# Performance work log

Hardware: AMD Instinct MI355X
Metric: run time of the kernel (lower is better)

The kernel has to match this reference:

```python
import jax, jax.numpy as jnp
import numpy as np

N = 50000
E = 800000
IN_DIM = 128
HIDDEN = 128
OUT_DIM = 64
NUM_GRAPHS = 64


def setup_inputs() -> dict:
    key = jax.random.key(0)
    ks = jax.random.split(key, 16)
    x = jax.random.normal(ks[0], (N, IN_DIM), dtype=jnp.float32)
    edge_index = jax.random.randint(ks[1], (2, E), 0, N, dtype=jnp.int32)
    batch = jnp.sort(jax.random.randint(ks[2], (N,), 0, NUM_GRAPHS, dtype=jnp.int32))

    def glorot(k, shape):
        fan_in = shape[1]
        return jax.random.normal(k, shape, dtype=jnp.float32) / jnp.sqrt(jnp.float32(fan_in))

    # SAGEConv params: lin_l (on aggregated neighbors, with bias), lin_r (on self, no bias)
    return {
        "x": x,
        "edge_index": edge_index,
        "batch": batch,
        "W1l": glorot(ks[3], (HIDDEN, IN_DIM)), "b1l": jnp.zeros((HIDDEN,), jnp.float32),
        "W1r": glorot(ks[4], (HIDDEN, IN_DIM)),
        "W2l": glorot(ks[5], (HIDDEN, HIDDEN)), "b2l": jnp.zeros((HIDDEN,), jnp.float32),
        "W2r": glorot(ks[6], (HIDDEN, HIDDEN)),
        "W3l": glorot(ks[7], (HIDDEN, HIDDEN)), "b3l": jnp.zeros((HIDDEN,), jnp.float32),
        "W3r": glorot(ks[8], (HIDDEN, HIDDEN)),
        "Wlin": glorot(ks[9], (OUT_DIM, HIDDEN)), "blin": jnp.zeros((OUT_DIM,), jnp.float32),
    }


def sage_conv(x, src, dst, Wl, bl, Wr):
    # aggr='add': scatter-add source features onto target nodes, then two linears.
    agg = jax.ops.segment_sum(x[src], dst, num_segments=N)  # [N, d_in]
    return agg @ Wl.T + bl + x @ Wr.T


def reference(x, edge_index, batch, W1l, b1l, W1r, W2l, b2l, W2r, W3l, b3l, W3r, Wlin, blin):
    src, dst = edge_index[0], edge_index[1]
    h = jax.nn.relu(sage_conv(x, src, dst, W1l, b1l, W1r))
    # dropout p=0.3 is identity at inference
    h = jax.nn.relu(sage_conv(h, src, dst, W2l, b2l, W2r))
    h = sage_conv(h, src, dst, W3l, b3l, W3r)
    # global mean pool over graphs
    sums = jax.ops.segment_sum(h, batch, num_segments=NUM_GRAPHS)  # [G, hidden]
    counts = jax.ops.segment_sum(jnp.ones((N,), h.dtype), batch, num_segments=NUM_GRAPHS)
    pooled = sums / jnp.maximum(counts, 1.0)[:, None]
    return pooled @ Wlin.T + blin  # [G, out_dim]
```

## Files before the change

kernel.cpp:

```cpp
#include <hip/hip_runtime.h>


typedef __bf16 bf16x8 __attribute__((ext_vector_type(8)));
typedef float f32x4 __attribute__((ext_vector_type(4)));
typedef float f32x2 __attribute__((ext_vector_type(2)));

#define BINB 160
#define NBMAX 512

static __device__ __forceinline__ float bf2f(unsigned short u) {
    union { unsigned u; float f; } c; c.u = (unsigned)u << 16; return c.f;
}
static __device__ __forceinline__ unsigned short f2bf(float f) {
    unsigned u = __builtin_bit_cast(unsigned, f);
    return (unsigned short)((u + 0x7fffu + ((u >> 16) & 1u)) >> 16);
}
static __device__ __forceinline__ uint2 pk8_fp8(const float* f) {
    int lo = 0, hi = 0;
    lo = __builtin_amdgcn_cvt_pk_fp8_f32(f[0], f[1], lo, false);
    lo = __builtin_amdgcn_cvt_pk_fp8_f32(f[2], f[3], lo, true);
    hi = __builtin_amdgcn_cvt_pk_fp8_f32(f[4], f[5], hi, false);
    hi = __builtin_amdgcn_cvt_pk_fp8_f32(f[6], f[7], hi, true);
    return make_uint2((unsigned)lo, (unsigned)hi);
}
static __device__ __forceinline__ unsigned char f2fp8(float v) {
    return (unsigned char)(__builtin_amdgcn_cvt_pk_fp8_f32(v, v, 0, false) & 0xff);
}

__global__ __launch_bounds__(256) void k_bincount(
    const int* __restrict__ dst, int* __restrict__ cnt_mat, int E, int nb, int epb)
{
    __shared__ int lc[NBMAX];
    for (int i = threadIdx.x; i < nb; i += 256) lc[i] = 0;
    __syncthreads();
    int b0 = blockIdx.x * epb;
    int b1 = min(b0 + epb, E);
    for (int i = b0 + threadIdx.x; i < b1; i += 256)
        atomicAdd(&lc[dst[i] >> 7], 1);
    __syncthreads();
    for (int i = threadIdx.x; i < nb; i += 256)
        cnt_mat[i * BINB + blockIdx.x] = lc[i];
}

__global__ __launch_bounds__(256) void k_mrowscan(
    const int* __restrict__ cnt_mat, int* __restrict__ rowloc, int* __restrict__ btot)
{
    __shared__ int s[256];
    int b = blockIdx.x;
    int t = threadIdx.x;
    int v = (t < BINB) ? cnt_mat[b * BINB + t] : 0;
    s[t] = v;
    __syncthreads();
#pragma unroll
    for (int off = 1; off < 256; off <<= 1) {
        int u = (t >= off) ? s[t - off] : 0;
        __syncthreads();
        s[t] += u;
        __syncthreads();
    }
    if (t < BINB) rowloc[b * BINB + t] = s[t] - v;
    if (t == 255) btot[b] = s[255];
}

__global__ __launch_bounds__(256) void k_scan2b(
    const int* __restrict__ btot, int* __restrict__ bbase, int nb, int* __restrict__ total_out)
{
    __shared__ int s[256];
    int t = threadIdx.x;
    int per = (nb + 255) / 256;
    int s0 = t * per, e0 = min(s0 + per, nb);
    int sum = 0;
    for (int i = s0; i < e0; ++i) sum += btot[i];
    s[t] = sum;
    __syncthreads();
#pragma unroll
    for (int off = 1; off < 256; off <<= 1) {
        int u = (t >= off) ? s[t - off] : 0;
        __syncthreads();
        s[t] += u;
        __syncthreads();
    }
    int run = s[t] - sum;
    for (int i = s0; i < e0; ++i) { bbase[i] = run; run += btot[i]; }
    if (t == 255) *total_out = s[255];
}

__global__ __launch_bounds__(256) void k_binscatter(
    const int* __restrict__ ei, const int* __restrict__ rowloc, const int* __restrict__ bbase,
    unsigned* __restrict__ binned, int E, int nb, int epb)
{
    __shared__ int lofs[NBMAX];
    __shared__ int lcnt[NBMAX];
    for (int i = threadIdx.x; i < nb; i += 256) {
        lofs[i] = rowloc[i * BINB + blockIdx.x] + bbase[i];
        lcnt[i] = 0;
    }
    __syncthreads();
    int b0 = blockIdx.x * epb;
    int b1 = min(b0 + epb, E);
    for (int i = b0 + threadIdx.x; i < b1; i += 256) {
        int s = ei[i];
        int d = ei[E + i];
        int b = d >> 7;
        int r = atomicAdd(&lcnt[b], 1);
        binned[lofs[b] + r] = (unsigned)s | ((unsigned)(d & 127) << 16);
    }
}

__global__ __launch_bounds__(256) void k_fillfine2(
    const unsigned* __restrict__ binned, const int* __restrict__ bbase,
    const int* __restrict__ batch, int* __restrict__ starts,
    unsigned short* __restrict__ csr_src, int* __restrict__ gestart,
    int E, int nb, int n)
{
    __shared__ int lc[128];
    __shared__ int lpos[128];
    int b = blockIdx.x;
    int t = threadIdx.x;
    int node0 = b << 7;
    int bs = bbase[b];
    int be = (b == nb - 1) ? E : bbase[b + 1];
    if (t < 128) lc[t] = 0;
    __syncthreads();
    for (int i = bs + t; i < be; i += 256)
        atomicAdd(&lc[(binned[i] >> 16) & 127], 1);
    __syncthreads();
    int v = (t < 128) ? lc[t] : 0;
    if (t < 128) lpos[t] = v;
    __syncthreads();
#pragma unroll
    for (int off = 1; off < 128; off <<= 1) {
        int u = (t >= off && t < 128) ? lpos[t - off] : 0;
        __syncthreads();
        if (t < 128) lpos[t] += u;
        __syncthreads();
    }
    int excl = (t < 128) ? (lpos[t] - v) : 0;
    __syncthreads();
    if (t < 128) {
        int node = node0 + t;
        if (node < n) {
            int st = bs + excl;
            starts[node] = st;
            int bc = batch[node];
            int bp = (node == 0) ? -1 : batch[node - 1];
            for (int g = bp + 1; g <= bc; ++g) gestart[g] = st;
            if (node == n - 1)
                for (int g = bc + 1; g <= 64; ++g) gestart[g] = E;
        }
        lpos[t] = bs + excl;
    }
    if (b == nb - 1 && t == 0) starts[n] = E;
    __syncthreads();
    for (int i = bs + t; i < be; i += 256) {
        unsigned e = binned[i];
        int slot = atomicAdd(&lpos[(e >> 16) & 127], 1);
        csr_src[slot] = (unsigned short)(e & 0xffffu);
    }
}

__global__ __launch_bounds__(256) void k_cast_all(
    const float* __restrict__ x, unsigned short* __restrict__ xb,
    unsigned char* __restrict__ x8, int n8, int nxblk,
    const float* __restrict__ W1l, const float* __restrict__ W1r,
    const float* __restrict__ W2l, const float* __restrict__ W2r,
    unsigned short* __restrict__ Whi)
{
    int bid = blockIdx.x;
    if (bid < nxblk) {
        int i = bid * 256 + threadIdx.x;
        if (i >= n8) return;
        float f[8];
        *(float4*)(f + 0) = *(const float4*)(x + (size_t)i * 8);
        *(float4*)(f + 4) = *(const float4*)(x + (size_t)i * 8 + 4);
        ushort4 oa, ob;
        oa.x = f2bf(f[0]); oa.y = f2bf(f[1]); oa.z = f2bf(f[2]); oa.w = f2bf(f[3]);
        ob.x = f2bf(f[4]); ob.y = f2bf(f[5]); ob.z = f2bf(f[6]); ob.w = f2bf(f[7]);
        int node = i >> 4, c = i & 15;
        size_t dst = (size_t)(node >> 4) * 2048 + (size_t)(c >> 2) * 512
                   + (size_t)((c & 3) * 16 + (node & 15)) * 8;
        *(ushort4*)(xb + dst) = oa;
        *(ushort4*)(xb + dst + 4) = ob;
        *(uint2*)(x8 + (size_t)i * 8) = pk8_fp8(f);
    } else {
        int wb = bid - nxblk;
        int layer = wb >> 7;
        int j = wb & 127;
        int k = threadIdx.x;
        const float* Wl = (layer == 0) ? W1l : W2l;
        const float* Wr = (layer == 0) ? W1r : W2r;
        float w = (k < 128) ? Wl[j * 128 + k] : Wr[j * 128 + k - 128];
        int js = j >> 4, mr = j & 15;
        int s = k >> 5, quad = (k >> 3) & 3, e = k & 7;
        size_t o = (size_t)layer * 32768
                 + ((size_t)(js * 8 + s) * 64 + quad * 16 + mr) * 8 + e;
        Whi[o] = f2bf(w);
    }
}

#define ACC8(v)                                                         \
    do {                                                                \
        f32x2 p0 = __builtin_amdgcn_cvt_pk_f32_fp8((v).x, false);       \
        f32x2 p1 = __builtin_amdgcn_cvt_pk_f32_fp8((v).x, true);        \
        f32x2 p2 = __builtin_amdgcn_cvt_pk_f32_fp8((v).y, false);       \
        f32x2 p3 = __builtin_amdgcn_cvt_pk_f32_fp8((v).y, true);        \
        a0 += p0.x; a1 += p0.y; a2 += p1.x; a3 += p1.y;                 \
        a4 += p2.x; a5 += p2.y; a6 += p3.x; a7 += p3.y;                 \
    } while (0)

#define ACC_SEG(sbeg, send)                                             \
    for (int base = (sbeg); base < (send); base += 64) {                \
        int cnt = min(64, (send) - base);                               \
        int idx = (base + lane < (send)) ? (int)csr[base + lane] : 0;   \
        int j = 0;                                                      \
        for (; j + 16 <= cnt; j += 16) {                                \
            int s0 = __shfl(idx, j + eg);                               \
            int s1 = __shfl(idx, j + 4 + eg);                           \
            int s2 = __shfl(idx, j + 8 + eg);                           \
            int s3 = __shfl(idx, j + 12 + eg);                          \
            uint2 v0 = *(const uint2*)(hrow + (size_t)s0 * 128);        \
            uint2 v1 = *(const uint2*)(hrow + (size_t)s1 * 128);        \
            uint2 v2 = *(const uint2*)(hrow + (size_t)s2 * 128);        \
            uint2 v3 = *(const uint2*)(hrow + (size_t)s3 * 128);        \
            ACC8(v0);                                                   \
            ACC8(v1);                                                   \
            ACC8(v2);                                                   \
            ACC8(v3);                                                   \
        }                                                               \
        for (; j + 8 <= cnt; j += 8) {                                  \
            int s0 = __shfl(idx, j + eg);                               \
            int s1 = __shfl(idx, j + 4 + eg);                           \
            uint2 v0 = *(const uint2*)(hrow + (size_t)s0 * 128);        \
            uint2 v1 = *(const uint2*)(hrow + (size_t)s1 * 128);        \
            ACC8(v0);                                                   \
            ACC8(v1);                                                   \
        }                                                               \
        for (; j + 4 <= cnt; j += 4) {                                  \
            int s0 = __shfl(idx, j + eg);                               \
            uint2 v0 = *(const uint2*)(hrow + (size_t)s0 * 128);        \
            ACC8(v0);                                                   \
        }                                                               \
        if (j < cnt) {                                                  \
            int k = j + eg;                                             \
            int sm = __shfl(idx, (k < cnt) ? k : (cnt - 1));            \
            uint2 v = *(const uint2*)(hrow + (size_t)sm * 128);         \
            if (k >= cnt) v = make_uint2(0u, 0u);                       \
            ACC8(v);                                                    \
        }                                                               \
    }

#define REDUCE8()                                                       \
    a0 += __shfl_xor(a0, 16); a0 += __shfl_xor(a0, 32);                 \
    a1 += __shfl_xor(a1, 16); a1 += __shfl_xor(a1, 32);                 \
    a2 += __shfl_xor(a2, 16); a2 += __shfl_xor(a2, 32);                 \
    a3 += __shfl_xor(a3, 16); a3 += __shfl_xor(a3, 32);                 \
    a4 += __shfl_xor(a4, 16); a4 += __shfl_xor(a4, 32);                 \
    a5 += __shfl_xor(a5, 16); a5 += __shfl_xor(a5, 32);                 \
    a6 += __shfl_xor(a6, 16); a6 += __shfl_xor(a6, 32);                 \
    a7 += __shfl_xor(a7, 16); a7 += __shfl_xor(a7, 32);

__global__ __launch_bounds__(256) void k_agg(
    const unsigned char* __restrict__ h8, const int* __restrict__ starts,
    const unsigned short* __restrict__ csr, unsigned short* __restrict__ aggf, int n)
{
    int node = blockIdx.x * 4 + (threadIdx.x >> 6);
    int lane = threadIdx.x & 63;
    if (node >= n) return;
    int eg = lane >> 4;
    int fb = lane & 15;
    const unsigned char* hrow = h8 + fb * 8;
    float a0 = 0.f, a1 = 0.f, a2 = 0.f, a3 = 0.f,
          a4 = 0.f, a5 = 0.f, a6 = 0.f, a7 = 0.f;
    int s = starts[node], e = starts[node + 1];

    ACC_SEG(s, e)
    REDUCE8()

    unsigned u0 = (unsigned)f2bf(a0) | ((unsigned)f2bf(a1) << 16);
    unsigned u1 = (unsigned)f2bf(a2) | ((unsigned)f2bf(a3) << 16);
    unsigned u2 = (unsigned)f2bf(a4) | ((unsigned)f2bf(a5) << 16);
    unsigned u3 = (unsigned)f2bf(a6) | ((unsigned)f2bf(a7) << 16);
    if (eg == 0) {
        size_t dst = (size_t)(node >> 4) * 2048 + (size_t)(fb >> 2) * 512
                   + (size_t)((fb & 3) * 16 + (node & 15)) * 8;
        *(uint4*)(aggf + dst) = make_uint4(u0, u1, u2, u3);
    }
}

__global__ __launch_bounds__(256) void k_tail(
    const unsigned char* __restrict__ h8, const unsigned short* __restrict__ csr,
    const int* __restrict__ gestart, float* __restrict__ gsumE,
    const int* __restrict__ batch, float* __restrict__ gsumP,
    int E, int n, int apgrid)
{
    __shared__ float gbuf[4][128];
    int t = threadIdx.x;
    if ((int)blockIdx.x >= apgrid) {
        int wave = ((blockIdx.x - apgrid) * 256 + t) >> 6;
        int lane = t & 63;
        int r0 = wave * 16;
        if (r0 >= n) return;
        int r1 = min(r0 + 16, n);
        int cur = batch[r0];
        float ax = 0.f, ay = 0.f;
        for (int i = r0; i < r1; ++i) {
            int g = batch[i];
            uchar2 v = *(const uchar2*)(h8 + (size_t)i * 128 + lane * 2);
            if (g != cur) {
                atomicAdd(&gsumP[cur * 128 + lane * 2], ax);
                atomicAdd(&gsumP[cur * 128 + lane * 2 + 1], ay);
                ax = 0.f; ay = 0.f; cur = g;
            }
            unsigned pk = (unsigned)v.x | ((unsigned)v.y << 8);
            f32x2 p = __builtin_amdgcn_cvt_pk_f32_fp8((int)pk, false);
            ax += p.x;
            ay += p.y;
        }
        atomicAdd(&gsumP[cur * 128 + lane * 2], ax);
        atomicAdd(&gsumP[cur * 128 + lane * 2 + 1], ay);
        return;
    }

    int B0 = blockIdx.x * 256;
    if (B0 >= E) return;
    for (int q = t; q < 512; q += 256) gbuf[q >> 7][q & 127] = 0.f;
    __syncthreads();

    int lo = 0, hi = 63;
    while (lo < hi) { int m = (lo + hi + 1) >> 1; if (gestart[m] <= B0) lo = m; else hi = m - 1; }
    int gblk = lo;

    int wv = t >> 6;
    int lane = t & 63;
    int e0 = B0 + wv * 64;
    if (e0 < E) {
        int e1 = min(e0 + 64, E);
        int eg = lane >> 4;
        int fb = lane & 15;
        const unsigned char* hrow = h8 + fb * 8;

        int g = gblk;
        while (g < 63 && gestart[g + 1] <= e0) ++g;

        float a0 = 0.f, a1 = 0.f, a2 = 0.f, a3 = 0.f,
              a4 = 0.f, a5 = 0.f, a6 = 0.f, a7 = 0.f;
        int cur = e0;
        bool dirty = false;
        while (cur < e1) {
            int gend = gestart[g + 1];
            int send = min(e1, gend);

            ACC_SEG(cur, send)
            dirty = true;
            cur = send;

            if (cur == gend) {
                REDUCE8()
                if (eg == 0) {
                    int gi = g - gblk;
                    if (gi < 4) {
                        float* d = &gbuf[gi][fb * 8];
                        atomicAdd(d + 0, a0); atomicAdd(d + 1, a1);
                        atomicAdd(d + 2, a2); atomicAdd(d + 3, a3);
                        atomicAdd(d + 4, a4); atomicAdd(d + 5, a5);
                        atomicAdd(d + 6, a6); atomicAdd(d + 7, a7);
                    } else {
                        float* d = &gsumE[(size_t)g * 128 + fb * 8];
                        atomicAdd(d + 0, a0); atomicAdd(d + 1, a1);
                        atomicAdd(d + 2, a2); atomicAdd(d + 3, a3);
                        atomicAdd(d + 4, a4); atomicAdd(d + 5, a5);
                        atomicAdd(d + 6, a6); atomicAdd(d + 7, a7);
                    }
                }
                a0 = a1 = a2 = a3 = a4 = a5 = a6 = a7 = 0.f;
                dirty = false;
                ++g;
                while (g < 63 && gestart[g + 1] <= cur) ++g;
            }
        }
        if (dirty) {
            REDUCE8()
            if (eg == 0) {
                int gi = g - gblk;
                if (gi < 4) {
                    float* d = &gbuf[gi][fb * 8];
                    atomicAdd(d + 0, a0); atomicAdd(d + 1, a1);
                    atomicAdd(d + 2, a2); atomicAdd(d + 3, a3);
                    atomicAdd(d + 4, a4); atomicAdd(d + 5, a5);
                    atomicAdd(d + 6, a6); atomicAdd(d + 7, a7);
                } else {
                    float* d = &gsumE[(size_t)g * 128 + fb * 8];
                    atomicAdd(d + 0, a0); atomicAdd(d + 1, a1);
                    atomicAdd(d + 2, a2); atomicAdd(d + 3, a3);
                    atomicAdd(d + 4, a4); atomicAdd(d + 5, a5);
                    atomicAdd(d + 6, a6); atomicAdd(d + 7, a7);
                }
            }
        }
    }
    __syncthreads();
    for (int q = t; q < 512; q += 256) {
        int sl = q >> 7, c = q & 127;
        float v = gbuf[sl][c];
        if (v != 0.f && gblk + sl < 64)
            atomicAdd(&gsumE[(size_t)(gblk + sl) * 128 + c], v);
    }
}

__global__ __launch_bounds__(256) void k_sage(
    const unsigned short* __restrict__ aggf, const unsigned short* __restrict__ hf,
    const unsigned short* __restrict__ Whi,
    const float* __restrict__ bl, unsigned short* __restrict__ outf,
    unsigned char* __restrict__ out8, int n, int do_relu, int do_outf)
{
    int bid = blockIdx.x;
    int pair = bid >> 1;
    int jh = bid & 1;
    int t = threadIdx.x;
    int wv = t >> 6;
    int l = t & 63;
    int quad = l >> 4;
    int mr = l & 15;
    int js = jh * 4 + wv;
    int jbase = js * 16;
    int nb0 = pair * 2;
    int node0 = pair * 32;

    f32x4 acc0 = (f32x4){0.f, 0.f, 0.f, 0.f};
    f32x4 acc1 = (f32x4){0.f, 0.f, 0.f, 0.f};

    const unsigned short* wp = Whi + (size_t)js * 4096 + (size_t)l * 8;

    uint4 pb[2][3];
#define SAGE_LOAD(s, b)                                                   \
    do {                                                                  \
        const unsigned short* ab = ((s) < 4)                              \
            ? (aggf + (size_t)(s) * 512 + (size_t)l * 8)                  \
            : (hf + (size_t)((s) - 4) * 512 + (size_t)l * 8);             \
        pb[b][0] = *(const uint4*)(wp + (size_t)(s) * 512);               \
        pb[b][1] = *(const uint4*)(ab + (size_t)nb0 * 2048);              \
        pb[b][2] = *(const uint4*)(ab + (size_t)(nb0 + 1) * 2048);        \
    } while (0)

    SAGE_LOAD(0, 0);
    SAGE_LOAD(1, 1);
#pragma unroll
    for (int s = 0; s < 8; ++s) {
        int b = s & 1;
        bf16x8 bh = __builtin_bit_cast(bf16x8, pb[b][0]);
        bf16x8 a0 = __builtin_bit_cast(bf16x8, pb[b][1]);
        bf16x8 a1 = __builtin_bit_cast(bf16x8, pb[b][2]);
        acc0 = __builtin_amdgcn_mfma_f32_16x16x32_bf16(a0, bh, acc0, 0, 0, 0);
        acc1 = __builtin_amdgcn_mfma_f32_16x16x32_bf16(a1, bh, acc1, 0, 0, 0);
        if (s + 2 < 8) SAGE_LOAD(s + 2, b);
    }
#undef SAGE_LOAD

    int col = jbase + mr;
    float bias = bl[col];
    int q2 = (col >> 3) & 3;
    int e2 = col & 7;
    int so = col >> 5;

#pragma unroll
    for (int mi = 0; mi < 2; ++mi) {
        f32x4 a = mi ? acc1 : acc0;
#pragma unroll
        for (int r = 0; r < 4; ++r) {
            int node = node0 + mi * 16 + quad * 4 + r;
            if (node >= n) continue;
            float v = a[r] + bias;
            if (do_relu) v = fmaxf(v, 0.f);
            if (do_outf)
                outf[(size_t)(node >> 4) * 2048 + (size_t)so * 512
                     + (size_t)(q2 * 16 + (node & 15)) * 8 + e2] = f2bf(v);
            out8[(size_t)node * 128 + col] = f2fp8(v);
        }
    }
}

__global__ __launch_bounds__(128) void k_final(
    const float* __restrict__ gsumE, const float* __restrict__ gsumP,
    const int* __restrict__ batch,
    const float* __restrict__ W3l, const float* __restrict__ b3,
    const float* __restrict__ W3r,
    const float* __restrict__ Wlin, const float* __restrict__ blin,
    float* __restrict__ out, int n)
{
    __shared__ float tmp[128];
    int g = blockIdx.x;
    int t = threadIdx.x;
    int lo = 0, hi = n;
    while (lo < hi) { int m = (lo + hi) >> 1; if (batch[m] < g) lo = m + 1; else hi = m; }
    int lb = lo;
    hi = n;
    while (lo < hi) { int m = (lo + hi) >> 1; if (batch[m] < g + 1) lo = m + 1; else hi = m; }
    int cnt = lo - lb;
    float inv = (cnt > 0) ? 1.f / (float)cnt : 0.f;

    float acc = 0.f;
    for (int k = 0; k < 128; ++k)
        acc += gsumE[g * 128 + k] * W3l[t * 128 + k]
             + gsumP[g * 128 + k] * W3r[t * 128 + k];
    tmp[t] = acc * inv + ((cnt > 0) ? b3[t] : 0.f);
    __syncthreads();

    if (t < 64) {
        float o = 0.f;
        for (int k = 0; k < 128; ++k)
            o += tmp[k] * Wlin[t * 128 + k];
        out[g * 64 + t] = o + blin[t];
    }
}

extern "C" void kernel_launch(void* const* d_in, const int* in_sizes, int n_in,
                              void* d_out, int out_size, void* d_ws, size_t ws_size,
                              hipStream_t stream) {
    const float* x     = (const float*)d_in[0];
    const int*   ei    = (const int*)d_in[1];
    const int*   batch = (const int*)d_in[2];
    const float* W1l = (const float*)d_in[3];
    const float* b1l = (const float*)d_in[4];
    const float* W1r = (const float*)d_in[5];
    const float* W2l = (const float*)d_in[6];
    const float* b2l = (const float*)d_in[7];
    const float* W2r = (const float*)d_in[8];
    const float* W3l = (const float*)d_in[9];
    const float* b3l = (const float*)d_in[10];
    const float* W3r = (const float*)d_in[11];
    const float* Wlin = (const float*)d_in[12];
    const float* blin = (const float*)d_in[13];

    const int N = in_sizes[2];
    const int E = in_sizes[1] / 2;
    const int nb = (N + 127) >> 7;
    const int epb = (E + BINB - 1) / BINB;

    size_t off = 0;
    auto alloc = [&](size_t bytes) {
        void* p = (char*)d_ws + off;
        off += (bytes + 255) & ~(size_t)255;
        return p;
    };
    int* csr_start = (int*)alloc((size_t)(N + 1) * 4);
    int* cnt_mat   = (int*)alloc((size_t)nb * BINB * 4);
    int* rowloc    = (int*)alloc((size_t)nb * BINB * 4);
    int* btot      = (int*)alloc((size_t)NBMAX * 4);
    int* bbase     = (int*)alloc((size_t)NBMAX * 4);
    int* gestart   = (int*)alloc(256 + 64);
    unsigned short* csr_src = (unsigned short*)alloc((size_t)E * 2);
    unsigned short* x_bf   = (unsigned short*)alloc((size_t)N * 128 * 2 + 65536);
    unsigned short* hA     = (unsigned short*)alloc((size_t)N * 128 * 2 + 65536);
    unsigned short* agg_bf = (unsigned short*)alloc((size_t)N * 128 * 2 + 65536);
    unsigned char*  h_f8   = (unsigned char*)alloc((size_t)N * 128);
    unsigned short* Whi = (unsigned short*)alloc(2 * 128 * 256 * 2);
    float* gsumE = (float*)alloc((size_t)64 * 128 * 4);
    float* gsumP = (float*)alloc((size_t)64 * 128 * 4);
    (void)ws_size;

    unsigned* binned = (unsigned*)agg_bf;

    hipMemsetAsync(gsumE, 0, (size_t)2 * 64 * 128 * 4, stream);

    k_bincount<<<BINB, 256, 0, stream>>>(ei + E, cnt_mat, E, nb, epb);
    k_mrowscan<<<nb, 256, 0, stream>>>(cnt_mat, rowloc, btot);
    k_scan2b<<<1, 256, 0, stream>>>(btot, bbase, nb, csr_start + N);
    k_binscatter<<<BINB, 256, 0, stream>>>(ei, rowloc, bbase, binned, E, nb, epb);
    k_fillfine2<<<nb, 256, 0, stream>>>(binned, bbase, batch, csr_start, csr_src,
                                        gestart, E, nb, N);

    int n8 = N * 128 / 8;
    int nxblk = (n8 + 255) / 256;
    k_cast_all<<<nxblk + 2 * 128, 256, 0, stream>>>(
        x, x_bf, h_f8, n8, nxblk, W1l, W1r, W2l, W2r, Whi);

    int agg_grid = (N + 3) / 4;
    int sage_grid = ((N + 31) / 32) * 2;
    int pool_grid = (((N + 15) / 16) + 3) / 4;
    int aggpool_grid = (E + 255) / 256;

    k_agg<<<agg_grid, 256, 0, stream>>>(h_f8, csr_start, csr_src, agg_bf, N);
    k_sage<<<sage_grid, 256, 0, stream>>>(agg_bf, x_bf, Whi, b1l,
                                          hA, h_f8, N, 1, 1);
    k_agg<<<agg_grid, 256, 0, stream>>>(h_f8, csr_start, csr_src, agg_bf, N);
    k_sage<<<sage_grid, 256, 0, stream>>>(agg_bf, hA, Whi + 32768, b2l,
                                          hA, h_f8, N, 1, 0);
    k_tail<<<aggpool_grid + pool_grid, 256, 0, stream>>>(
        h_f8, csr_src, gestart, gsumE, batch, gsumP, E, N, aggpool_grid);

    k_final<<<64, 128, 0, stream>>>(gsumE, gsumP, batch, W3l, b3l, W3r,
                                    Wlin, blin, (float*)d_out, N);
}
```

Before: 246.2 us.

## Fuse neighbor aggregation into SAGE matmul kernel and merge bincount with cast

```diff
diff --git a/kernel.cpp b/kernel.cpp
--- a/kernel.cpp
+++ b/kernel.cpp
@@ -27,19 +27,55 @@
     return (unsigned char)(__builtin_amdgcn_cvt_pk_fp8_f32(v, v, 0, false) & 0xff);
 }
 
-__global__ __launch_bounds__(256) void k_bincount(
-    const int* __restrict__ dst, int* __restrict__ cnt_mat, int E, int nb, int epb)
+__global__ __launch_bounds__(256) void k_bincast(
+    const int* __restrict__ dst, int* __restrict__ cnt_mat, int E, int nb, int epb,
+    const float* __restrict__ x, unsigned short* __restrict__ xb,
+    unsigned char* __restrict__ x8, int n8, int nxblk,
+    const float* __restrict__ W1l, const float* __restrict__ W1r,
+    const float* __restrict__ W2l, const float* __restrict__ W2r,
+    unsigned short* __restrict__ Whi)
 {
     __shared__ int lc[NBMAX];
-    for (int i = threadIdx.x; i < nb; i += 256) lc[i] = 0;
-    __syncthreads();
-    int b0 = blockIdx.x * epb;
-    int b1 = min(b0 + epb, E);
-    for (int i = b0 + threadIdx.x; i < b1; i += 256)
-        atomicAdd(&lc[dst[i] >> 7], 1);
-    __syncthreads();
-    for (int i = threadIdx.x; i < nb; i += 256)
-        cnt_mat[i * BINB + blockIdx.x] = lc[i];
+    int bid = blockIdx.x;
+    if (bid < BINB) {
+        for (int i = threadIdx.x; i < nb; i += 256) lc[i] = 0;
+        __syncthreads();
+        int b0 = bid * epb;
+        int b1 = min(b0 + epb, E);
+        for (int i = b0 + threadIdx.x; i < b1; i += 256)
+            atomicAdd(&lc[dst[i] >> 7], 1);
+        __syncthreads();
+        for (int i = threadIdx.x; i < nb; i += 256)
+            cnt_mat[i * BINB + bid] = lc[i];
+    } else if (bid < BINB + nxblk) {
+        int i = (bid - BINB) * 256 + threadIdx.x;
+        if (i >= n8) return;
+        float f[8];
+        *(float4*)(f + 0) = *(const float4*)(x + (size_t)i * 8);
+        *(float4*)(f + 4) = *(const float4*)(x + (size_t)i * 8 + 4);
+        ushort4 oa, ob;
+        oa.x = f2bf(f[0]); oa.y = f2bf(f[1]); oa.z = f2bf(f[2]); oa.w = f2bf(f[3]);
+        ob.x = f2bf(f[4]); ob.y = f2bf(f[5]); ob.z = f2bf(f[6]); ob.w = f2bf(f[7]);
+        int node = i >> 4, c = i & 15;
+        size_t dstb = (size_t)(node >> 4) * 2048 + (size_t)(c >> 2) * 512
+                    + (size_t)((c & 3) * 16 + (node & 15)) * 8;
+        *(ushort4*)(xb + dstb) = oa;
+        *(ushort4*)(xb + dstb + 4) = ob;
+        *(uint2*)(x8 + (size_t)i * 8) = pk8_fp8(f);
+    } else {
+        int wb = bid - BINB - nxblk;
+        int layer = wb >> 7;
+        int j = wb & 127;
+        int k = threadIdx.x;
+        const float* Wl = (layer == 0) ? W1l : W2l;
+        const float* Wr = (layer == 0) ? W1r : W2r;
+        float w = (k < 128) ? Wl[j * 128 + k] : Wr[j * 128 + k - 128];
+        int js = j >> 4, mr = j & 15;
+        int s = k >> 5, quad = (k >> 3) & 3, e = k & 7;
+        size_t o = (size_t)layer * 32768
+                 + ((size_t)(js * 8 + s) * 64 + quad * 16 + mr) * 8 + e;
+        Whi[o] = f2bf(w);
+    }
 }
 
 __global__ __launch_bounds__(256) void k_mrowscan(
@@ -156,45 +192,6 @@
         unsigned e = binned[i];
         int slot = atomicAdd(&lpos[(e >> 16) & 127], 1);
         csr_src[slot] = (unsigned short)(e & 0xffffu);
-    }
-}
-
-__global__ __launch_bounds__(256) void k_cast_all(
-    const float* __restrict__ x, unsigned short* __restrict__ xb,
-    unsigned char* __restrict__ x8, int n8, int nxblk,
-    const float* __restrict__ W1l, const float* __restrict__ W1r,
-    const float* __restrict__ W2l, const float* __restrict__ W2r,
-    unsigned short* __restrict__ Whi)
-{
-    int bid = blockIdx.x;
-    if (bid < nxblk) {
-        int i = bid * 256 + threadIdx.x;
-        if (i >= n8) return;
-        float f[8];
-        *(float4*)(f + 0) = *(const float4*)(x + (size_t)i * 8);
-        *(float4*)(f + 4) = *(const float4*)(x + (size_t)i * 8 + 4);
-        ushort4 oa, ob;
-        oa.x = f2bf(f[0]); oa.y = f2bf(f[1]); oa.z = f2bf(f[2]); oa.w = f2bf(f[3]);
-        ob.x = f2bf(f[4]); ob.y = f2bf(f[5]); ob.z = f2bf(f[6]); ob.w = f2bf(f[7]);
-        int node = i >> 4, c = i & 15;
-        size_t dst = (size_t)(node >> 4) * 2048 + (size_t)(c >> 2) * 512
-                   + (size_t)((c & 3) * 16 + (node & 15)) * 8;
-        *(ushort4*)(xb + dst) = oa;
-        *(ushort4*)(xb + dst + 4) = ob;
-        *(uint2*)(x8 + (size_t)i * 8) = pk8_fp8(f);
-    } else {
-        int wb = bid - nxblk;
-        int layer = wb >> 7;
-        int j = wb & 127;
-        int k = threadIdx.x;
-        const float* Wl = (layer == 0) ? W1l : W2l;
-        const float* Wr = (layer == 0) ? W1r : W2r;
-        float w = (k < 128) ? Wl[j * 128 + k] : Wr[j * 128 + k - 128];
-        int js = j >> 4, mr = j & 15;
-        int s = k >> 5, quad = (k >> 3) & 3, e = k & 7;
-        size_t o = (size_t)layer * 32768
-                 + ((size_t)(js * 8 + s) * 64 + quad * 16 + mr) * 8 + e;
-        Whi[o] = f2bf(w);
     }
 }
 
@@ -259,31 +256,107 @@
     a6 += __shfl_xor(a6, 16); a6 += __shfl_xor(a6, 32);                 \
     a7 += __shfl_xor(a7, 16); a7 += __shfl_xor(a7, 32);
 
-__global__ __launch_bounds__(256) void k_agg(
-    const unsigned char* __restrict__ h8, const int* __restrict__ starts,
-    const unsigned short* __restrict__ csr, unsigned short* __restrict__ aggf, int n)
-{
-    int node = blockIdx.x * 4 + (threadIdx.x >> 6);
-    int lane = threadIdx.x & 63;
-    if (node >= n) return;
-    int eg = lane >> 4;
-    int fb = lane & 15;
-    const unsigned char* hrow = h8 + fb * 8;
-    float a0 = 0.f, a1 = 0.f, a2 = 0.f, a3 = 0.f,
-          a4 = 0.f, a5 = 0.f, a6 = 0.f, a7 = 0.f;
-    int s = starts[node], e = starts[node + 1];
-
-    ACC_SEG(s, e)
-    REDUCE8()
-
-    unsigned u0 = (unsigned)f2bf(a0) | ((unsigned)f2bf(a1) << 16);
-    unsigned u1 = (unsigned)f2bf(a2) | ((unsigned)f2bf(a3) << 16);
-    unsigned u2 = (unsigned)f2bf(a4) | ((unsigned)f2bf(a5) << 16);
-    unsigned u3 = (unsigned)f2bf(a6) | ((unsigned)f2bf(a7) << 16);
-    if (eg == 0) {
-        size_t dst = (size_t)(node >> 4) * 2048 + (size_t)(fb >> 2) * 512
-                   + (size_t)((fb & 3) * 16 + (node & 15)) * 8;
-        *(uint4*)(aggf + dst) = make_uint4(u0, u1, u2, u3);
+__global__ __launch_bounds__(512) void k_layer(
+    const unsigned char* __restrict__ h8_in, const int* __restrict__ starts,
+    const unsigned short* __restrict__ csr, const unsigned short* __restrict__ hf,
+    const unsigned short* __restrict__ Whi, const float* __restrict__ bl,
+    unsigned short* __restrict__ outf, unsigned char* __restrict__ out8,
+    int n, int do_relu, int do_outf)
+{
+    __shared__ unsigned short sagg[4096];
+    int t = threadIdx.x;
+    int wv = t >> 6;
+    int lane = t & 63;
+    int node0 = blockIdx.x * 32;
+
+    {
+        int eg = lane >> 4;
+        int fb = lane & 15;
+        const unsigned char* hrow = h8_in + fb * 8;
+        for (int r = 0; r < 4; ++r) {
+            int node = node0 + wv * 4 + r;
+            if (node >= n) break;
+            float a0 = 0.f, a1 = 0.f, a2 = 0.f, a3 = 0.f,
+                  a4 = 0.f, a5 = 0.f, a6 = 0.f, a7 = 0.f;
+            int s = starts[node], e = starts[node + 1];
+
+            ACC_SEG(s, e)
+            REDUCE8()
+
+            if (eg == 0) {
+                int ln = node - node0;
+                unsigned u0 = (unsigned)f2bf(a0) | ((unsigned)f2bf(a1) << 16);
+                unsigned u1 = (unsigned)f2bf(a2) | ((unsigned)f2bf(a3) << 16);
+                unsigned u2 = (unsigned)f2bf(a4) | ((unsigned)f2bf(a5) << 16);
+                unsigned u3 = (unsigned)f2bf(a6) | ((unsigned)f2bf(a7) << 16);
+                size_t dst = (size_t)(ln >> 4) * 2048 + (size_t)(fb >> 2) * 512
+                           + (size_t)((fb & 3) * 16 + (ln & 15)) * 8;
+                *(uint4*)(sagg + dst) = make_uint4(u0, u1, u2, u3);
+            }
+        }
+    }
+    __syncthreads();
+
+    int quad = lane >> 4;
+    int mr = lane & 15;
+    int js = wv;
+    int jbase = js * 16;
+    size_t nb0 = (size_t)blockIdx.x * 2;
+
+    f32x4 acc0 = (f32x4){0.f, 0.f, 0.f, 0.f};
+    f32x4 acc1 = (f32x4){0.f, 0.f, 0.f, 0.f};
+
+    const unsigned short* wp = Whi + (size_t)js * 4096 + (size_t)lane * 8;
+    const unsigned short* sa = sagg + (size_t)lane * 8;
+    const unsigned short* ha = hf + nb0 * 2048 + (size_t)lane * 8;
+
+    uint4 pb[2][3];
+#define LAYER_LOAD(s, b)                                                  \
+    do {                                                                  \
+        pb[b][0] = *(const uint4*)(wp + (size_t)(s) * 512);               \
+        if ((s) < 4) {                                                    \
+            pb[b][1] = *(const uint4*)(sa + (size_t)(s) * 512);           \
+            pb[b][2] = *(const uint4*)(sa + (size_t)(s) * 512 + 2048);    \
+        } else {                                                          \
+            pb[b][1] = *(const uint4*)(ha + (size_t)((s) - 4) * 512);     \
+            pb[b][2] = *(const uint4*)(ha + (size_t)((s) - 4) * 512 + 2048); \
+        }                                                                 \
+    } while (0)
+
+    LAYER_LOAD(0, 0);
+    LAYER_LOAD(1, 1);
+#pragma unroll
+    for (int s = 0; s < 8; ++s) {
+        int b = s & 1;
+        bf16x8 bh = __builtin_bit_cast(bf16x8, pb[b][0]);
+        bf16x8 A0 = __builtin_bit_cast(bf16x8, pb[b][1]);
+        bf16x8 A1 = __builtin_bit_cast(bf16x8, pb[b][2]);
+        acc0 = __builtin_amdgcn_mfma_f32_16x16x32_bf16(A0, bh, acc0, 0, 0, 0);
+        acc1 = __builtin_amdgcn_mfma_f32_16x16x32_bf16(A1, bh, acc1, 0, 0, 0);
+        if (s + 2 < 8) LAYER_LOAD(s + 2, b);
+    }
+#undef LAYER_LOAD
+
+    int col = jbase + mr;
+    float bias = bl[col];
+    int q2 = (col >> 3) & 3;
+    int e2 = col & 7;
+    int so = col >> 5;
+
+#pragma unroll
+    for (int mi = 0; mi < 2; ++mi) {
+        f32x4 a = mi ? acc1 : acc0;
+#pragma unroll
+        for (int r = 0; r < 4; ++r) {
+            int node = node0 + mi * 16 + quad * 4 + r;
+            if (node >= n) continue;
+            float v = a[r] + bias;
+            if (do_relu) v = fmaxf(v, 0.f);
+            if (do_outf)
+                outf[(size_t)(node >> 4) * 2048 + (size_t)so * 512
+                     + (size_t)(q2 * 16 + (node & 15)) * 8 + e2] = f2bf(v);
+            out8[(size_t)node * 128 + col] = f2fp8(v);
+        }
     }
 }
 
@@ -407,78 +480,6 @@
     }
 }
 
-__global__ __launch_bounds__(256) void k_sage(
-    const unsigned short* __restrict__ aggf, const unsigned short* __restrict__ hf,
-    const unsigned short* __restrict__ Whi,
-    const float* __restrict__ bl, unsigned short* __restrict__ outf,
-    unsigned char* __restrict__ out8, int n, int do_relu, int do_outf)
-{
-    int bid = blockIdx.x;
-    int pair = bid >> 1;
-    int jh = bid & 1;
-    int t = threadIdx.x;
-    int wv = t >> 6;
-    int l = t & 63;
-    int quad = l >> 4;
-    int mr = l & 15;
-    int js = jh * 4 + wv;
-    int jbase = js * 16;
-    int nb0 = pair * 2;
-    int node0 = pair * 32;
-
-    f32x4 acc0 = (f32x4){0.f, 0.f, 0.f, 0.f};
-    f32x4 acc1 = (f32x4){0.f, 0.f, 0.f, 0.f};
-
-    const unsigned short* wp = Whi + (size_t)js * 4096 + (size_t)l * 8;
-
-    uint4 pb[2][3];
-#define SAGE_LOAD(s, b)                                                   \
-    do {                                                                  \
-        const unsigned short* ab = ((s) < 4)                              \
-            ? (aggf + (size_t)(s) * 512 + (size_t)l * 8)                  \
-            : (hf + (size_t)((s) - 4) * 512 + (size_t)l * 8);             \
-        pb[b][0] = *(const uint4*)(wp + (size_t)(s) * 512);               \
-        pb[b][1] = *(const uint4*)(ab + (size_t)nb0 * 2048);              \
-        pb[b][2] = *(const uint4*)(ab + (size_t)(nb0 + 1) * 2048);        \
-    } while (0)
-
-    SAGE_LOAD(0, 0);
-    SAGE_LOAD(1, 1);
-#pragma unroll
-    for (int s = 0; s < 8; ++s) {
-        int b = s & 1;
-        bf16x8 bh = __builtin_bit_cast(bf16x8, pb[b][0]);
-        bf16x8 a0 = __builtin_bit_cast(bf16x8, pb[b][1]);
-        bf16x8 a1 = __builtin_bit_cast(bf16x8, pb[b][2]);
-        acc0 = __builtin_amdgcn_mfma_f32_16x16x32_bf16(a0, bh, acc0, 0, 0, 0);
-        acc1 = __builtin_amdgcn_mfma_f32_16x16x32_bf16(a1, bh, acc1, 0, 0, 0);
-        if (s + 2 < 8) SAGE_LOAD(s + 2, b);
-    }
-#undef SAGE_LOAD
-
-    int col = jbase + mr;
-    float bias = bl[col];
-    int q2 = (col >> 3) & 3;
-    int e2 = col & 7;
-    int so = col >> 5;
-
-#pragma unroll
-    for (int mi = 0; mi < 2; ++mi) {
-        f32x4 a = mi ? acc1 : acc0;
-#pragma unroll
-        for (int r = 0; r < 4; ++r) {
-            int node = node0 + mi * 16 + quad * 4 + r;
-            if (node >= n) continue;
-            float v = a[r] + bias;
-            if (do_relu) v = fmaxf(v, 0.f);
-            if (do_outf)
-                outf[(size_t)(node >> 4) * 2048 + (size_t)so * 512
-                     + (size_t)(q2 * 16 + (node & 15)) * 8 + e2] = f2bf(v);
-            out8[(size_t)node * 128 + col] = f2fp8(v);
-        }
-    }
-}
-
 __global__ __launch_bounds__(128) void k_final(
     const float* __restrict__ gsumE, const float* __restrict__ gsumP,
     const int* __restrict__ batch,
@@ -549,44 +550,40 @@
     int* bbase     = (int*)alloc((size_t)NBMAX * 4);
     int* gestart   = (int*)alloc(256 + 64);
     unsigned short* csr_src = (unsigned short*)alloc((size_t)E * 2);
-    unsigned short* x_bf   = (unsigned short*)alloc((size_t)N * 128 * 2 + 65536);
-    unsigned short* hA     = (unsigned short*)alloc((size_t)N * 128 * 2 + 65536);
-    unsigned short* agg_bf = (unsigned short*)alloc((size_t)N * 128 * 2 + 65536);
-    unsigned char*  h_f8   = (unsigned char*)alloc((size_t)N * 128);
+    unsigned*       binned  = (unsigned*)alloc((size_t)E * 4);
+    unsigned short* x_bf = (unsigned short*)alloc((size_t)N * 128 * 2 + 65536);
+    unsigned short* hA   = (unsigned short*)alloc((size_t)N * 128 * 2 + 65536);
+    unsigned char*  x8   = (unsigned char*)alloc((size_t)N * 128);
+    unsigned char*  h1_8 = (unsigned char*)alloc((size_t)N * 128);
+    unsigned char*  h2_8 = (unsigned char*)alloc((size_t)N * 128);
     unsigned short* Whi = (unsigned short*)alloc(2 * 128 * 256 * 2);
     float* gsumE = (float*)alloc((size_t)64 * 128 * 4);
     float* gsumP = (float*)alloc((size_t)64 * 128 * 4);
     (void)ws_size;
 
-    unsigned* binned = (unsigned*)agg_bf;
-
     hipMemsetAsync(gsumE, 0, (size_t)2 * 64 * 128 * 4, stream);
 
-    k_bincount<<<BINB, 256, 0, stream>>>(ei + E, cnt_mat, E, nb, epb);
+    int n8 = N * 128 / 8;
+    int nxblk = (n8 + 255) / 256;
+    k_bincast<<<BINB + nxblk + 256, 256, 0, stream>>>(
+        ei + E, cnt_mat, E, nb, epb,
+        x, x_bf, x8, n8, nxblk, W1l, W1r, W2l, W2r, Whi);
     k_mrowscan<<<nb, 256, 0, stream>>>(cnt_mat, rowloc, btot);
     k_scan2b<<<1, 256, 0, stream>>>(btot, bbase, nb, csr_start + N);
     k_binscatter<<<BINB, 256, 0, stream>>>(ei, rowloc, bbase, binned, E, nb, epb);
     k_fillfine2<<<nb, 256, 0, stream>>>(binned, bbase, batch, csr_start, csr_src,
                                         gestart, E, nb, N);
 
-    int n8 = N * 128 / 8;
-    int nxblk = (n8 + 255) / 256;
-    k_cast_all<<<nxblk + 2 * 128, 256, 0, stream>>>(
-        x, x_bf, h_f8, n8, nxblk, W1l, W1r, W2l, W2r, Whi);
-
-    int agg_grid = (N + 3) / 4;
-    int sage_grid = ((N + 31) / 32) * 2;
+    int lay_grid = (N + 31) / 32;
     int pool_grid = (((N + 15) / 16) + 3) / 4;
     int aggpool_grid = (E + 255) / 256;
 
-    k_agg<<<agg_grid, 256, 0, stream>>>(h_f8, csr_start, csr_src, agg_bf, N);
-    k_sage<<<sage_grid, 256, 0, stream>>>(agg_bf, x_bf, Whi, b1l,
-                                          hA, h_f8, N, 1, 1);
-    k_agg<<<agg_grid, 256, 0, stream>>>(h_f8, csr_start, csr_src, agg_bf, N);
-    k_sage<<<sage_grid, 256, 0, stream>>>(agg_bf, hA, Whi + 32768, b2l,
-                                          hA, h_f8, N, 1, 0);
+    k_layer<<<lay_grid, 512, 0, stream>>>(x8, csr_start, csr_src, x_bf,
+                                          Whi, b1l, hA, h1_8, N, 1, 1);
+    k_layer<<<lay_grid, 512, 0, stream>>>(h1_8, csr_start, csr_src, hA,
+                                          Whi + 32768, b2l, hA, h2_8, N, 1, 0);
     k_tail<<<aggpool_grid + pool_grid, 256, 0, stream>>>(
-        h_f8, csr_src, gestart, gsumE, batch, gsumP, E, N, aggpool_grid);
+        h2_8, csr_src, gestart, gsumE, batch, gsumP, E, N, aggpool_grid);
 
     k_final<<<64, 128, 0, stream>>>(gsumE, gsumP, batch, W3l, b3l, W3r,
                                     Wlin, blin, (float*)d_out, N);
```

Result: no change. 244.5 us (-0.7%).
